# Kernel optimization log

Measured on AMD Instinct MI355X. Metric: run time of the kernel, lower is better.

## Reference

```python
import jax, jax.numpy as jnp
import numpy as np

OUT_FEATURES = 4096
IN_FEATURES = 4096
K = 4096
BLOCK_SIZE = 8
NUM_BLOCKS = OUT_FEATURES * IN_FEATURES // BLOCK_SIZE  # 2,097,152
ORIGINAL_NUMEL = OUT_FEATURES * IN_FEATURES


def setup_inputs() -> dict:
    key = jax.random.key(0)
    k1, k2, k3, k4 = jax.random.split(key, 4)
    x = jax.random.normal(k1, (4, 2048, IN_FEATURES), dtype=jnp.float32)
    codebook = jax.random.normal(k2, (K, BLOCK_SIZE), dtype=jnp.float32)
    indices = jax.random.randint(k3, (NUM_BLOCKS,), 0, K, dtype=jnp.int64)
    bias = jax.random.normal(k4, (OUT_FEATURES,), dtype=jnp.float32)
    return {"x": x, "codebook": codebook, "indices": indices, "bias": bias}


def reference(x, codebook, indices, bias):
    # Reconstruct weight from codebook: gather blocks, flatten, slice, reshape.
    reconstructed = codebook[indices]                      # [num_blocks, block_size]
    W = reconstructed.reshape(-1)[:ORIGINAL_NUMEL]
    W = W.reshape(OUT_FEATURES, IN_FEATURES)               # [out, in]
    # F.linear: x @ W^T + bias
    return jnp.einsum('bsi,oi->bso', x, W) + bias
```

## Files before the change

### kernel.cpp

```cpp
#include <hip/hip_runtime.h>
#include <stdint.h>


#define M_DIM 8192
#define N_DIM 4096
#define K_DIM 4096
#define BM 128
#define BN 128
#define BK 32
#define NUM_W_BLOCKS 2097152
#define W_WGS (NUM_W_BLOCKS / 256)
#define X_THREADS (M_DIM * K_DIM / 16)
#define X_WGS (X_THREADS / 256)

typedef __attribute__((ext_vector_type(8))) __bf16 bf16x8;
typedef __attribute__((ext_vector_type(4))) float floatx4;

__device__ __forceinline__ unsigned int f2bf(float f) {
    unsigned int u = __builtin_bit_cast(unsigned int, f);
    u += 0x7fffu + ((u >> 16) & 1u);
    return u >> 16;
}

__device__ __forceinline__ uint4 pack8(float4 a, float4 c) {
    uint4 o;
    o.x = f2bf(a.x) | (f2bf(a.y) << 16);
    o.y = f2bf(a.z) | (f2bf(a.w) << 16);
    o.z = f2bf(c.x) | (f2bf(c.y) << 16);
    o.w = f2bf(c.z) | (f2bf(c.w) << 16);
    return o;
}

__global__ __launch_bounds__(256) void prep_kernel(
    const float* __restrict__ cb, const int* __restrict__ idx,
    uint4* __restrict__ W, const float4* __restrict__ x,
    uint4* __restrict__ xb) {
    const int wg = blockIdx.x;
    if (wg < W_WGS) {
        const int b = wg * 256 + threadIdx.x;
        const int id = idx[b];
        const float4* s = (const float4*)(cb + ((size_t)id << 3));
        W[b] = pack8(s[0], s[1]);
    } else {
        const size_t t = (size_t)(wg - W_WGS) * 256 + threadIdx.x;
        const float4* src = x + 4 * t;
        const float4 a = src[0], b = src[1], c = src[2], d = src[3];
        uint4* dst = xb + 2 * t;
        dst[0] = pack8(a, b);
        dst[1] = pack8(c, d);
    }
}

__device__ __forceinline__ void async_copy16(const void* g, void* s) {
    __builtin_amdgcn_global_load_lds(
        (const __attribute__((address_space(1))) unsigned int*)(uintptr_t)g,
        (__attribute__((address_space(3))) unsigned int*)(uintptr_t)s,
        16, 0, 0);
}

__global__ __launch_bounds__(256) void gemm_bt_kernel(
    const __bf16* __restrict__ A,
    const __bf16* __restrict__ B,
    const float* __restrict__ bias,
    float* __restrict__ C) {
    __shared__ __align__(16) __bf16 sA[BM * BK];
    __shared__ __align__(16) __bf16 sB[BN * BK];

    const int tid = threadIdx.x;
    const int wave = tid >> 6;
    const int lane = tid & 63;

    const int m0 = blockIdx.x * BM;
    const int n0 = blockIdx.y * BN;

    const int wm = (wave >> 1) * 64;
    const int wn = (wave & 1) * 64;

    const int fr = lane & 15;
    const int fk = (lane >> 4) * 8;

    const int srow = tid >> 2;
    const int scol = (tid & 3) * 8;

    const __bf16* gA = A + (size_t)(m0 + srow) * K_DIM + scol;
    const __bf16* gB = B + (size_t)(n0 + srow) * K_DIM + scol;
    __bf16* sAw = sA + wave * 512;
    __bf16* sBw = sB + wave * 512;

    floatx4 acc[4][4] = {};

    for (int k0 = 0; k0 < K_DIM; k0 += BK) {
        async_copy16(gA + k0, sAw);
        async_copy16(gA + k0 + (size_t)64 * K_DIM, sAw + 2048);
        async_copy16(gB + k0, sBw);
        async_copy16(gB + k0 + (size_t)64 * K_DIM, sBw + 2048);
        __syncthreads();

        bf16x8 af[4], bfr[4];
#pragma unroll
        for (int i = 0; i < 4; ++i)
            af[i] = *(const bf16x8*)(sA + (wm + i * 16 + fr) * BK + fk);
#pragma unroll
        for (int j = 0; j < 4; ++j)
            bfr[j] = *(const bf16x8*)(sB + (wn + j * 16 + fr) * BK + fk);

#pragma unroll
        for (int i = 0; i < 4; ++i)
#pragma unroll
            for (int j = 0; j < 4; ++j)
                acc[i][j] = __builtin_amdgcn_mfma_f32_16x16x32_bf16(
                    af[i], bfr[j], acc[i][j], 0, 0, 0);
        __syncthreads();
    }

    const int crow = (lane >> 4) * 4;
    const int ccol = lane & 15;
#pragma unroll
    for (int j = 0; j < 4; ++j) {
        const int n = n0 + wn + j * 16 + ccol;
        const float bv = bias[n];
#pragma unroll
        for (int i = 0; i < 4; ++i) {
            const int m = m0 + wm + i * 16 + crow;
            float* cp = C + (size_t)m * N_DIM + n;
#pragma unroll
            for (int r = 0; r < 4; ++r)
                __builtin_nontemporal_store(acc[i][j][r] + bv,
                                            cp + (size_t)r * N_DIM);
        }
    }
}

extern "C" void kernel_launch(void* const* d_in, const int* in_sizes, int n_in,
                              void* d_out, int out_size, void* d_ws, size_t ws_size,
                              hipStream_t stream) {
    const float* x    = (const float*)d_in[0];
    const float* cb   = (const float*)d_in[1];
    const int*   idx  = (const int*)d_in[2];
    const float* bias = (const float*)d_in[3];
    float* out = (float*)d_out;

    __bf16* Wb = (__bf16*)d_ws;
    __bf16* Xb = (__bf16*)((char*)d_ws + (size_t)N_DIM * K_DIM * sizeof(__bf16));

    prep_kernel<<<W_WGS + X_WGS, 256, 0, stream>>>(
        cb, idx, (uint4*)Wb, (const float4*)x, (uint4*)Xb);

    dim3 grid(M_DIM / BM, N_DIM / BN);
    gemm_bt_kernel<<<grid, 256, 0, stream>>>(Xb, Wb, bias, out);
}
```

Measured before the change: 550.8 us.

## Swizzle LDS tile layout and use one-float4-per-thread nontemporal conversion

Applies an XOR swizzle to the k-chunk position of each row in the shared-memory A/B tiles. The swizzle is applied both when the async global-to-LDS copies are issued and when MFMA fragments are read, with the aim of reducing LDS bank conflicts. The x fp32-to-bf16 conversion now handles one float4 per thread with coalesced nontemporal loads instead of four, which quadruples the number of prep workgroups. The index load also becomes nontemporal. The swizzle must match on the write and read sides to stay correct.

```diff
diff --git a/kernel.cpp b/kernel.cpp
--- a/kernel.cpp
+++ b/kernel.cpp
@@ -10,11 +10,11 @@
 #define BK 32
 #define NUM_W_BLOCKS 2097152
 #define W_WGS (NUM_W_BLOCKS / 256)
-#define X_THREADS (M_DIM * K_DIM / 16)
-#define X_WGS (X_THREADS / 256)
+#define X_WGS ((M_DIM * K_DIM / 4) / 256)
 
 typedef __attribute__((ext_vector_type(8))) __bf16 bf16x8;
 typedef __attribute__((ext_vector_type(4))) float floatx4;
+typedef __attribute__((ext_vector_type(2))) unsigned int uintx2;
 
 __device__ __forceinline__ unsigned int f2bf(float f) {
     unsigned int u = __builtin_bit_cast(unsigned int, f);
@@ -22,32 +22,30 @@
     return u >> 16;
 }
 
-__device__ __forceinline__ uint4 pack8(float4 a, float4 c) {
-    uint4 o;
-    o.x = f2bf(a.x) | (f2bf(a.y) << 16);
-    o.y = f2bf(a.z) | (f2bf(a.w) << 16);
-    o.z = f2bf(c.x) | (f2bf(c.y) << 16);
-    o.w = f2bf(c.z) | (f2bf(c.w) << 16);
-    return o;
-}
-
 __global__ __launch_bounds__(256) void prep_kernel(
     const float* __restrict__ cb, const int* __restrict__ idx,
-    uint4* __restrict__ W, const float4* __restrict__ x,
-    uint4* __restrict__ xb) {
+    uint4* __restrict__ W, const floatx4* __restrict__ x,
+    uintx2* __restrict__ xb) {
     const int wg = blockIdx.x;
     if (wg < W_WGS) {
         const int b = wg * 256 + threadIdx.x;
-        const int id = idx[b];
+        const int id = __builtin_nontemporal_load(idx + b);
         const float4* s = (const float4*)(cb + ((size_t)id << 3));
-        W[b] = pack8(s[0], s[1]);
+        const float4 a = s[0];
+        const float4 c = s[1];
+        uint4 o;
+        o.x = f2bf(a.x) | (f2bf(a.y) << 16);
+        o.y = f2bf(a.z) | (f2bf(a.w) << 16);
+        o.z = f2bf(c.x) | (f2bf(c.y) << 16);
+        o.w = f2bf(c.z) | (f2bf(c.w) << 16);
+        W[b] = o;
     } else {
         const size_t t = (size_t)(wg - W_WGS) * 256 + threadIdx.x;
-        const float4* src = x + 4 * t;
-        const float4 a = src[0], b = src[1], c = src[2], d = src[3];
-        uint4* dst = xb + 2 * t;
-        dst[0] = pack8(a, b);
-        dst[1] = pack8(c, d);
+        const floatx4 a = __builtin_nontemporal_load(x + t);
+        uintx2 o;
+        o.x = f2bf(a.x) | (f2bf(a.y) << 16);
+        o.y = f2bf(a.z) | (f2bf(a.w) << 16);
+        xb[t] = o;
     }
 }
 
@@ -77,10 +75,10 @@
     const int wn = (wave & 1) * 64;
 
     const int fr = lane & 15;
-    const int fk = (lane >> 4) * 8;
+    const int sw = (((lane >> 4) ^ ((fr >> 1) & 3)) * 8);
 
     const int srow = tid >> 2;
-    const int scol = (tid & 3) * 8;
+    const int scol = ((tid & 3) ^ ((srow >> 1) & 3)) * 8;
 
     const __bf16* gA = A + (size_t)(m0 + srow) * K_DIM + scol;
     const __bf16* gB = B + (size_t)(n0 + srow) * K_DIM + scol;
@@ -99,10 +97,10 @@
         bf16x8 af[4], bfr[4];
 #pragma unroll
         for (int i = 0; i < 4; ++i)
-            af[i] = *(const bf16x8*)(sA + (wm + i * 16 + fr) * BK + fk);
+            af[i] = *(const bf16x8*)(sA + (wm + i * 16 + fr) * BK + sw);
 #pragma unroll
         for (int j = 0; j < 4; ++j)
-            bfr[j] = *(const bf16x8*)(sB + (wn + j * 16 + fr) * BK + fk);
+            bfr[j] = *(const bf16x8*)(sB + (wn + j * 16 + fr) * BK + sw);
 
 #pragma unroll
         for (int i = 0; i < 4; ++i)
@@ -144,7 +142,7 @@
     __bf16* Xb = (__bf16*)((char*)d_ws + (size_t)N_DIM * K_DIM * sizeof(__bf16));
 
     prep_kernel<<<W_WGS + X_WGS, 256, 0, stream>>>(
-        cb, idx, (uint4*)Wb, (const float4*)x, (uint4*)Xb);
+        cb, idx, (uint4*)Wb, (const floatx4*)x, (uintx2*)Xb);
 
     dim3 grid(M_DIM / BM, N_DIM / BN);
     gemm_bt_kernel<<<grid, 256, 0, stream>>>(Xb, Wb, bias, out);
```

Result: faster. 529.0 us (-4.0%).
